# Kernel optimization log

Measured on AMD Instinct MI355X. Metric: run time of the kernel, lower is better.

## Reference

```python
import jax, jax.numpy as jnp
import numpy as np

N, D, H, E = 50000, 128, 128, 800000


def setup_inputs() -> dict:
    key = jax.random.key(0)
    ks = jax.random.split(key, 12)
    p = lambda k, shape: jax.random.normal(k, shape, dtype=jnp.float32) * 0.02
    z = lambda n: jnp.zeros((n,), jnp.float32)
    return {
        "x1": jax.random.normal(ks[0], (N, D), dtype=jnp.float32),
        "edge_index1": jax.random.randint(ks[1], (2, E), 0, N, dtype=jnp.int32),
        "x2": jax.random.normal(ks[2], (N, D), dtype=jnp.float32),
        "edge_index2": jax.random.randint(ks[3], (2, E), 0, N, dtype=jnp.int32),
        "enc_w1": p(ks[4], (D, H)), "enc_b1": z(H),
        "enc_w2": p(ks[5], (H, H)), "enc_b2": z(H),
        "conv1_w": p(ks[6], (H, H)), "conv1_b": z(H),
        "conv2_w": p(ks[7], (H, H)), "conv2_b": z(H),
        "sim_w1": p(ks[8], (4 * H, H)), "sim_b1": z(H),
        "sim_w2": p(ks[9], (H, 1)), "sim_b2": z(1),
    }


def reference(x1, edge_index1, x2, edge_index2,
              enc_w1, enc_b1, enc_w2, enc_b2,
              conv1_w, conv1_b, conv2_w, conv2_b,
              sim_w1, sim_b1, sim_w2, sim_b2):
    def gcn(x, ei, W, b):
        row, col = ei[0], ei[1]            # [E], [E]
        h = x @ W + b                      # [N, H]
        n = x.shape[0]
        deg = jax.ops.segment_sum(jnp.ones(row.shape[0], h.dtype), row, num_segments=n)
        dis = jnp.where(deg > 0, deg ** -0.5, 0.0)   # deg^-0.5, inf -> 0
        norm = dis[row] * dis[col]         # [E]
        msg = h[col] * norm[:, None]       # gather + per-edge scale, [E, H]
        return jax.ops.segment_sum(msg, row, num_segments=n)  # scatter-add

    def embed(x, ei):
        h = jax.nn.relu(x @ enc_w1 + enc_b1) @ enc_w2 + enc_b2  # encoder MLP
        h = jax.nn.relu(gcn(h, ei, conv1_w, conv1_b))
        h = jax.nn.relu(gcn(h, ei, conv2_w, conv2_b))
        return h.mean(axis=0)              # mean pooling -> [H]

    g1 = embed(x1, edge_index1)
    g2 = embed(x2, edge_index2)
    c = jnp.concatenate([g1, g2, jnp.abs(g1 - g2), g1 * g2], axis=-1)  # [4H]
    return jax.nn.relu(c @ sim_w1 + sim_b1) @ sim_w2 + sim_b2          # [1]
```

## Files before the change

kernel.cpp:

```cpp
#include <hip/hip_runtime.h>

#define HD 128

typedef _Float16 f16x8 __attribute__((ext_vector_type(8)));
typedef _Float16 f16x2 __attribute__((ext_vector_type(2)));
typedef float f32x4 __attribute__((ext_vector_type(4)));

template<bool RELU, bool SCALE, bool CVT, bool WF16>
__device__ __forceinline__ void gemm_block(
    _Float16* lds, int bi,
    const _Float16* __restrict__ Ab, const float* __restrict__ Af0,
    const float* __restrict__ Af1, const void* __restrict__ Wsrc,
    const float* __restrict__ bias, const float* __restrict__ scale,
    _Float16* __restrict__ C, int N, int Ntot) {
  const int tid = threadIdx.x;
  if (WF16) {
    const _Float16* Wf = (const _Float16*)Wsrc;
    #pragma unroll
    for (int i = 0; i < 8; ++i)
      *(float4*)&lds[tid * 8 + i * 2048] = *(const float4*)&Wf[tid * 8 + i * 2048];
  } else {
    const float* Wg = (const float*)Wsrc;
    #pragma unroll
    for (int i = 0; i < 16; ++i) {
      int flat = i * 1024 + tid * 4;
      int k = flat >> 7, n0 = flat & 127;
      float4 w4 = *(const float4*)(Wg + flat);
      int kc = k >> 5, q = (k >> 3) & 3, j = k & 7;
      float wv[4] = {w4.x, w4.y, w4.z, w4.w};
      #pragma unroll
      for (int d = 0; d < 4; ++d) {
        int n = n0 + d;
        lds[(size_t)(((n >> 4) * 4 + kc) * 64 + 16 * q + (n & 15)) * 8 + j] = (_Float16)wv[d];
      }
    }
  }
  __syncthreads();

  const int lane = tid & 63;
  const int wave = tid >> 6;
  const int n16 = lane & 15, q = lane >> 4;
  const int rowbase = bi * 128 + wave * 32;

  int arow[2];
  #pragma unroll
  for (int t = 0; t < 2; ++t) {
    int r = rowbase + 16 * t + n16;
    arow[t] = (r < Ntot) ? r : (Ntot - 1);
  }

  f32x4 acc[2][8];
  #pragma unroll
  for (int t = 0; t < 2; ++t)
    #pragma unroll
    for (int nt = 0; nt < 8; ++nt) acc[t][nt] = (f32x4){0.f, 0.f, 0.f, 0.f};

  #pragma unroll
  for (int kc = 0; kc < 4; ++kc) {
    f16x8 a[2];
    #pragma unroll
    for (int t = 0; t < 2; ++t) {
      if (CVT) {
        int r = arow[t];
        const float* src = (r < N) ? (Af0 + (size_t)r * HD) : (Af1 + (size_t)(r - N) * HD);
        float4 u0 = *(const float4*)(src + kc * 32 + q * 8);
        float4 u1 = *(const float4*)(src + kc * 32 + q * 8 + 4);
        union { _Float16 h[8]; f16x8 v; } tmp;
        tmp.h[0] = (_Float16)u0.x; tmp.h[1] = (_Float16)u0.y;
        tmp.h[2] = (_Float16)u0.z; tmp.h[3] = (_Float16)u0.w;
        tmp.h[4] = (_Float16)u1.x; tmp.h[5] = (_Float16)u1.y;
        tmp.h[6] = (_Float16)u1.z; tmp.h[7] = (_Float16)u1.w;
        a[t] = tmp.v;
      } else {
        a[t] = *(const f16x8*)(Ab + (size_t)arow[t] * HD + kc * 32 + q * 8);
      }
    }
    #pragma unroll
    for (int nt = 0; nt < 8; ++nt) {
      f16x8 b = *(const f16x8*)&lds[(size_t)((nt * 4 + kc) * 64 + lane) * 8];
      #pragma unroll
      for (int t = 0; t < 2; ++t)
        acc[t][nt] = __builtin_amdgcn_mfma_f32_16x16x32_f16(a[t], b, acc[t][nt], 0, 0, 0);
    }
  }

  float bv[8];
  #pragma unroll
  for (int nt = 0; nt < 8; ++nt) bv[nt] = bias[nt * 16 + n16];

  #pragma unroll
  for (int t = 0; t < 2; ++t) {
    #pragma unroll
    for (int r = 0; r < 4; ++r) {
      int row = rowbase + 16 * t + 4 * q + r;
      if (row < Ntot) {
        float s = SCALE ? scale[row] : 1.0f;
        #pragma unroll
        for (int nt = 0; nt < 8; ++nt) {
          float v = acc[t][nt][r] + bv[nt];
          if (RELU) v = fmaxf(v, 0.f);
          if (SCALE) v *= s;
          C[(size_t)row * HD + nt * 16 + n16] = (_Float16)v;
        }
      }
    }
  }
}

template<bool RELU, bool SCALE, bool CVT, bool WF16, int AUX, int PAT>
__global__ __launch_bounds__(256, 4) void k_fused(
    const _Float16* __restrict__ Ab, const float* __restrict__ Af0,
    const float* __restrict__ Af1, const void* __restrict__ Wsrc,
    const float* __restrict__ bias, const float* __restrict__ scale,
    _Float16* __restrict__ C, int N, int Ntot, int G, int A,
    const int* __restrict__ ei0, const int* __restrict__ ei1, int E,
    int* __restrict__ deg2, unsigned short* __restrict__ slot,
    const float* __restrict__ w1, const float* __restrict__ w2,
    const float* __restrict__ w3, _Float16* __restrict__ WfOut, int degB,
    int* __restrict__ offs, int* __restrict__ partials,
    float* __restrict__ dis, int scanB,
    unsigned short* __restrict__ csr_col, int fillB, int* __restrict__ ctr) {
  __shared__ _Float16 lds[16384];
  __shared__ int lastFlag;
  const int bi = blockIdx.x;
  const int t = threadIdx.x;

  int role, rid;
  if (PAT == 2) { role = 0; rid = bi; }
  else if (PAT == 0) {
    if (bi < 3 * G) { int k = bi / 3, r = bi % 3;
      if (r == 2) { role = 0; rid = k; } else { role = 1; rid = 2 * k + r; } }
    else { role = 1; rid = bi - G; }
  } else {
    if (bi < 3 * A) { int k = bi / 3, r = bi % 3;
      if (r == 2) { role = 1; rid = k; } else { role = 0; rid = 2 * k + r; } }
    else { role = 0; rid = bi - A; }
  }

  if (role == 0) {
    gemm_block<RELU, SCALE, CVT, WF16>(lds, rid, Ab, Af0, Af1, Wsrc,
                                       bias, scale, C, N, Ntot);
    return;
  }

  if (AUX == 1) {
    if (rid < 2 * degB) {
      int g = (rid >= degB);
      int cb = rid - g * degB;
      const int* rows = g ? ei1 : ei0;
      int* deg = deg2 + g * N;
      unsigned short* sl = slot + (size_t)g * E;
      int base = (cb * 256 + t) * 4;
      if (base + 3 < E) {
        int4 r = *(const int4*)(rows + base);
        union { unsigned short us[4]; uint2 v; } s;
        s.us[0] = (unsigned short)atomicAdd(&deg[r.x], 1);
        s.us[1] = (unsigned short)atomicAdd(&deg[r.y], 1);
        s.us[2] = (unsigned short)atomicAdd(&deg[r.z], 1);
        s.us[3] = (unsigned short)atomicAdd(&deg[r.w], 1);
        *(uint2*)(sl + base) = s.v;
      } else {
        for (int e = base; e < E; ++e)
          sl[e] = (unsigned short)atomicAdd(&deg[rows[e]], 1);
      }
    } else {
      int wb = rid - 2 * degB;
      int m = wb >> 3;
      const float* Wg = (m == 0) ? w1 : (m == 1) ? w2 : w3;
      int idx0 = (wb & 7) * 2048 + t * 8;
      float4 u0 = *(const float4*)(Wg + idx0);
      float4 u1 = *(const float4*)(Wg + idx0 + 4);
      int k = idx0 >> 7, n0 = idx0 & 127;
      int kc = k >> 5, q2 = (k >> 3) & 3, j = k & 7;
      _Float16* dst = WfOut + (size_t)m * 16384;
      float vv[8] = {u0.x, u0.y, u0.z, u0.w, u1.x, u1.y, u1.z, u1.w};
      #pragma unroll
      for (int d = 0; d < 8; ++d) {
        int n = n0 + d;
        dst[(size_t)(((n >> 4) * 4 + kc) * 64 + 16 * q2 + (n & 15)) * 8 + j] = (_Float16)vv[d];
      }
    }
  } else if (AUX == 2) {
    int* s = (int*)lds;
    int i = rid * 256 + t;
    int v = (i < Ntot) ? deg2[i] : 0;
    s[t] = v;
    __syncthreads();
    #pragma unroll
    for (int off = 1; off < 256; off <<= 1) {
      int x = (t >= off) ? s[t - off] : 0;
      __syncthreads();
      s[t] += x;
      __syncthreads();
    }
    if (i < Ntot) {
      offs[i] = s[t] - v;
      dis[i] = (v > 0) ? (1.0f / sqrtf((float)v)) : 0.0f;
    }
    if (t == 255) partials[rid] = s[255];
    __syncthreads();
    if (t == 0) {
      __threadfence();
      lastFlag = (atomicAdd(ctr, 1) == scanB - 1);
    }
    __syncthreads();
    if (lastFlag) {
      __threadfence();
      volatile int* vp = partials;
      int P = scanB;
      int v0 = (t < P) ? vp[t] : 0;
      int v1 = (t + 256 < P) ? vp[t + 256] : 0;
      __syncthreads();
      s[t] = v0;
      s[t + 256] = v1;
      __syncthreads();
      #pragma unroll
      for (int off = 1; off < 256; off <<= 1) {
        int x0 = (t >= off) ? s[t - off] : 0;
        int x1 = (t >= off) ? s[256 + t - off] : 0;
        __syncthreads();
        s[t] += x0;
        s[256 + t] += x1;
        __syncthreads();
      }
      int tot0 = s[255];
      if (t < P) partials[t] = s[t] - v0;
      if (t + 256 < P) partials[t + 256] = s[256 + t] + tot0 - v1;
    }
  } else if (AUX == 4) {
    int g = (rid >= fillB);
    int cb = rid - g * fillB;
    const int* eg = (g ? ei1 : ei0);
    const int* ob = offs + g * N;
    const unsigned short* sl = slot + (size_t)g * E;
    int gN = g * N;
    int base = (cb * 256 + t) * 4;
    if (base + 3 < E) {
      int4 r = *(const int4*)(eg + base);
      int4 c = *(const int4*)(eg + E + base);
      uint2 sv = *(const uint2*)(sl + base);
      csr_col[ob[r.x] + partials[(gN + r.x) >> 8] + (sv.x & 0xffff)] = (unsigned short)c.x;
      csr_col[ob[r.y] + partials[(gN + r.y) >> 8] + (sv.x >> 16)]    = (unsigned short)c.y;
      csr_col[ob[r.z] + partials[(gN + r.z) >> 8] + (sv.y & 0xffff)] = (unsigned short)c.z;
      csr_col[ob[r.w] + partials[(gN + r.w) >> 8] + (sv.y >> 16)]    = (unsigned short)c.w;
    } else {
      for (int e = base; e < E; ++e)
        csr_col[ob[eg[e]] + partials[(gN + eg[e]) >> 8] + sl[e]] = (unsigned short)eg[E + e];
    }
  }
}

template<bool POOL>
__global__ __launch_bounds__(256) void k_aggregate(
    const _Float16* __restrict__ T, const int* __restrict__ offs,
    const int* __restrict__ partials, const unsigned short* __restrict__ csr_col,
    const float* __restrict__ dis, _Float16* __restrict__ out,
    float* __restrict__ poolrep, int N, int Ntot, int Etot) {
  __shared__ float red[4][128];
  const int lane = threadIdx.x & 63;
  const int wave = threadIdx.x >> 6;
  const int gw = blockIdx.x * 4 + wave;
  const int sub = lane >> 4, c16 = lane & 15;

  f16x2 hacc[4];
  #pragma unroll
  for (int j = 0; j < 4; ++j) hacc[j] = (f16x2){(_Float16)0.f, (_Float16)0.f};

  if (gw < Ntot) {
    const int beg = offs[gw] + partials[gw >> 8];
    const int end = (gw + 1 == Ntot) ? Etot : (offs[gw + 1] + partials[(gw + 1) >> 8]);
    const uint4* Tg = (const uint4*)(T + (size_t)(gw >= N ? N : 0) * HD);
    for (int e = beg; e < end; e += 16) {
      uint4 v[4];
      #pragma unroll
      for (int gp = 0; gp < 4; ++gp) {
        v[gp] = make_uint4(0, 0, 0, 0);
        if (e + 4 * gp < end) {
          int eg = e + 4 * gp + sub;
          bool valid = (eg < end);
          int ce = valid ? eg : (end - 1);
          int col = csr_col[ce];
          uint4 tv = Tg[(size_t)col * 16 + c16];
          if (valid) v[gp] = tv;
        }
      }
      #pragma unroll
      for (int gp = 0; gp < 4; ++gp) {
        union { uint4 u; f16x2 h[4]; } w;
        w.u = v[gp];
        hacc[0] += w.h[0];
        hacc[1] += w.h[1];
        hacc[2] += w.h[2];
        hacc[3] += w.h[3];
      }
    }
  }

  float ax[8];
  #pragma unroll
  for (int j = 0; j < 4; ++j) {
    ax[2 * j]     = (float)hacc[j][0];
    ax[2 * j + 1] = (float)hacc[j][1];
  }
  #pragma unroll
  for (int j = 0; j < 8; ++j) {
    ax[j] += __shfl_xor(ax[j], 32, 64);
    ax[j] += __shfl_xor(ax[j], 16, 64);
  }
  float dr = (gw < Ntot) ? dis[gw] : 0.f;
  #pragma unroll
  for (int j = 0; j < 8; ++j) ax[j] = fmaxf(ax[j] * dr, 0.f);

  if (!POOL) {
    if (gw < Ntot && sub == 0) {
      union { uint4 u; _Float16 h[8]; } o;
      #pragma unroll
      for (int j = 0; j < 8; ++j) o.h[j] = (_Float16)ax[j];
      ((uint4*)out)[(size_t)gw * 16 + c16] = o.u;
    }
  } else {
    if (sub == 0) {
      *(float4*)&red[wave][c16 * 8]     = make_float4(ax[0], ax[1], ax[2], ax[3]);
      *(float4*)&red[wave][c16 * 8 + 4] = make_float4(ax[4], ax[5], ax[6], ax[7]);
    }
    __syncthreads();
    int t = threadIdx.x;
    if (t < 128) {
      float s = red[0][t] + red[1][t] + red[2][t] + red[3][t];
      int g = (blockIdx.x * 4 >= N) ? 1 : 0;
      atomicAdd(&poolrep[(size_t)((blockIdx.x & 15) * 2 + g) * 128 + t], s);
    }
  }
}

__global__ void k_final(const float* __restrict__ poolrep,
                        const float* __restrict__ W1, const float* __restrict__ b1,
                        const float* __restrict__ W2, const float* __restrict__ b2,
                        float* __restrict__ out, float invN) {
  __shared__ float cs[512];
  __shared__ float red[2];
  int t = threadIdx.x;
  float g1 = 0.f, g2 = 0.f;
  #pragma unroll
  for (int r = 0; r < 16; ++r) {
    g1 += poolrep[r * 256 + t];
    g2 += poolrep[r * 256 + 128 + t];
  }
  g1 *= invN;
  g2 *= invN;
  cs[t] = g1;
  cs[128 + t] = g2;
  cs[256 + t] = fabsf(g1 - g2);
  cs[384 + t] = g1 * g2;
  __syncthreads();
  float acc = b1[t];
  #pragma unroll 8
  for (int i = 0; i < 512; ++i) acc = fmaf(cs[i], W1[(size_t)i * HD + t], acc);
  float h = fmaxf(acc, 0.f);
  float v = h * W2[t];
  #pragma unroll
  for (int off = 32; off > 0; off >>= 1) v += __shfl_down(v, off, 64);
  if ((t & 63) == 0) red[t >> 6] = v;
  __syncthreads();
  if (t == 0) out[0] = red[0] + red[1] + b2[0];
}

extern "C" void kernel_launch(void* const* d_in, const int* in_sizes, int n_in,
                              void* d_out, int out_size, void* d_ws, size_t ws_size,
                              hipStream_t stream) {
  const float* x1     = (const float*)d_in[0];
  const int*   ei1    = (const int*)d_in[1];
  const float* x2     = (const float*)d_in[2];
  const int*   ei2    = (const int*)d_in[3];
  const float* W_in[4] = {(const float*)d_in[4], (const float*)d_in[6],
                          (const float*)d_in[8], (const float*)d_in[10]};
  const float* B_in[4] = {(const float*)d_in[5], (const float*)d_in[7],
                          (const float*)d_in[9], (const float*)d_in[11]};
  const float* sim_w1 = (const float*)d_in[12];
  const float* sim_b1 = (const float*)d_in[13];
  const float* sim_w2 = (const float*)d_in[14];
  const float* sim_b2 = (const float*)d_in[15];

  const int N = in_sizes[0] / HD;
  const int E = in_sizes[1] / 2;
  const int Ntot = 2 * N;

  _Float16* sp = (_Float16*)d_ws;
  _Float16* bufA = sp; sp += (size_t)Ntot * HD;
  _Float16* bufB = sp; sp += (size_t)Ntot * HD;
  _Float16* WfB  = sp; sp += 3 * 16384;
  float* fp = (float*)sp;
  float* dis     = fp; fp += Ntot;
  float* poolrep = fp; fp += 16 * 256;
  int* ip = (int*)fp;
  int* ctrs     = ip; ip += 8;
  int* deg2     = ip; ip += Ntot;
  int* offs     = ip; ip += Ntot;
  int* partials = ip; ip += 512;
  ip = (int*)(((uintptr_t)ip + 15) & ~(uintptr_t)15);
  unsigned short* slot = (unsigned short*)ip;
  unsigned short* csr_col = slot + 2 * (size_t)E;

  const int G = (Ntot + 127) / 128;
  const int scanB = (Ntot + 255) / 256;
  const int aggB  = (Ntot + 3) / 4;
  const int degB  = ((E + 3) / 4 + 255) / 256;
  const int fillB = degB;

  hipMemsetAsync(poolrep, 0, (16 * 256 + 8 + Ntot) * sizeof(float), stream);

  {
    int A = 2 * degB + 24;
    k_fused<true, false, true, false, 1, 0><<<A + G, 256, 0, stream>>>(
        nullptr, x1, x2, W_in[0], B_in[0], nullptr, bufA, N, Ntot, G, A,
        ei1, ei2, E, deg2, slot, W_in[1], W_in[2], W_in[3], WfB, degB,
        offs, partials, dis, scanB, csr_col, fillB, ctrs);
  }
  k_fused<false, false, false, true, 2, 1><<<scanB + G, 256, 0, stream>>>(
      bufA, nullptr, nullptr, WfB + 0 * 16384, B_in[1], nullptr, bufB, N, Ntot, G, scanB,
      ei1, ei2, E, deg2, slot, nullptr, nullptr, nullptr, nullptr, degB,
      offs, partials, dis, scanB, csr_col, fillB, ctrs);
  k_fused<false, true, false, true, 4, 0><<<2 * fillB + G, 256, 0, stream>>>(
      bufB, nullptr, nullptr, WfB + 1 * 16384, B_in[2], dis, bufA, N, Ntot, G, 2 * fillB,
      ei1, ei2, E, deg2, slot, nullptr, nullptr, nullptr, nullptr, degB,
      offs, partials, dis, scanB, csr_col, fillB, ctrs);
  k_aggregate<false><<<aggB, 256, 0, stream>>>(
      bufA, offs, partials, csr_col, dis, bufB, nullptr, N, Ntot, 2 * E);
  k_fused<false, true, false, true, 0, 2><<<G, 256, 0, stream>>>(
      bufB, nullptr, nullptr, WfB + 2 * 16384, B_in[3], dis, bufA, N, Ntot, G, 0,
      ei1, ei2, E, deg2, slot, nullptr, nullptr, nullptr, nullptr, degB,
      offs, partials, dis, scanB, csr_col, fillB, ctrs);
  k_aggregate<true><<<aggB, 256, 0, stream>>>(
      bufA, offs, partials, csr_col, dis, nullptr, poolrep, N, Ntot, 2 * E);
  k_final<<<1, 128, 0, stream>>>(poolrep, sim_w1, sim_b1, sim_w2, sim_b2,
                                 (float*)d_out, 1.0f / (float)N);
}
```

Before: 409.3 us.

## Fuse encoder MLP chain and pipeline graph halves across fused role-mapped kernels

Fuses the two encoder layers into one kernel that keeps the intermediate activations in LDS per wave, removing a full global round trip. The work is restructured so that graph 1 and graph 2 are staggered. CSR fill for one graph overlaps with aggregation of the other, and each half's GEMM overlaps with the other half's aggregation, spread over several mixed-role kernels. This adds a third activation buffer, more launches, and a fairly intricate cross-kernel dependency schedule, including assumptions such as aggB = N/4 that require N to be divisible by 4.

```diff
diff --git a/kernel.cpp b/kernel.cpp
--- a/kernel.cpp
+++ b/kernel.cpp
@@ -6,41 +6,91 @@
 typedef _Float16 f16x2 __attribute__((ext_vector_type(2)));
 typedef float f32x4 __attribute__((ext_vector_type(4)));
 
-template<bool RELU, bool SCALE, bool CVT, bool WF16>
-__device__ __forceinline__ void gemm_block(
-    _Float16* lds, int bi,
-    const _Float16* __restrict__ Ab, const float* __restrict__ Af0,
-    const float* __restrict__ Af1, const void* __restrict__ Wsrc,
+__device__ __forceinline__ void role_map(int bi, int S, int k, int& role, int& rid) {
+  int q = bi / k, rem = bi - q * k;
+  if (rem == 0 && q < S) { role = 1; rid = q; }
+  else { role = 0; int na = q + (rem ? 1 : 0); if (na > S) na = S; rid = bi - na; }
+}
+
+__global__ void k_wcvt(const float* __restrict__ w0, const float* __restrict__ w1,
+                       const float* __restrict__ w2, const float* __restrict__ w3,
+                       _Float16* __restrict__ Wf) {
+  int m = blockIdx.x >> 3;
+  const float* Wg = (m == 0) ? w0 : (m == 1) ? w1 : (m == 2) ? w2 : w3;
+  int idx0 = (blockIdx.x & 7) * 2048 + threadIdx.x * 8;
+  float4 u0 = *(const float4*)(Wg + idx0);
+  float4 u1 = *(const float4*)(Wg + idx0 + 4);
+  int k = idx0 >> 7, n0 = idx0 & 127;
+  int kc = k >> 5, q2 = (k >> 3) & 3, j = k & 7;
+  _Float16* dst = Wf + (size_t)m * 16384;
+  float vv[8] = {u0.x, u0.y, u0.z, u0.w, u1.x, u1.y, u1.z, u1.w};
+  #pragma unroll
+  for (int d = 0; d < 8; ++d) {
+    int n = n0 + d;
+    dst[(size_t)(((n >> 4) * 4 + kc) * 64 + 16 * q2 + (n & 15)) * 8 + j] = (_Float16)vv[d];
+  }
+}
+
+__device__ __forceinline__ void deg_core(int rid, int degB,
+    const int* __restrict__ ei0, const int* __restrict__ ei1, int E, int N,
+    int* __restrict__ deg2, unsigned short* __restrict__ slot) {
+  int g = (rid >= degB);
+  int cb = rid - g * degB;
+  const int* rows = g ? ei1 : ei0;
+  int* deg = deg2 + g * N;
+  unsigned short* sl = slot + (size_t)g * E;
+  int base = (cb * 256 + threadIdx.x) * 4;
+  if (base + 3 < E) {
+    int4 r = *(const int4*)(rows + base);
+    union { unsigned short us[4]; uint2 v; } s;
+    s.us[0] = (unsigned short)atomicAdd(&deg[r.x], 1);
+    s.us[1] = (unsigned short)atomicAdd(&deg[r.y], 1);
+    s.us[2] = (unsigned short)atomicAdd(&deg[r.z], 1);
+    s.us[3] = (unsigned short)atomicAdd(&deg[r.w], 1);
+    *(uint2*)(sl + base) = s.v;
+  } else {
+    for (int e = base; e < E; ++e)
+      sl[e] = (unsigned short)atomicAdd(&deg[rows[e]], 1);
+  }
+}
+
+__device__ __forceinline__ void fill_core(int rid, int g,
+    const int* __restrict__ ei0, const int* __restrict__ ei1, int E, int N,
+    const int* __restrict__ offs, const int* __restrict__ partials,
+    const unsigned short* __restrict__ slot, unsigned short* __restrict__ csr_col) {
+  const int* eg = (g ? ei1 : ei0);
+  const int* ob = offs + g * N;
+  const unsigned short* sl = slot + (size_t)g * E;
+  int gN = g * N;
+  int base = (rid * 256 + threadIdx.x) * 4;
+  if (base + 3 < E) {
+    int4 r = *(const int4*)(eg + base);
+    int4 c = *(const int4*)(eg + E + base);
+    uint2 sv = *(const uint2*)(sl + base);
+    csr_col[ob[r.x] + partials[(gN + r.x) >> 8] + (sv.x & 0xffff)] = (unsigned short)c.x;
+    csr_col[ob[r.y] + partials[(gN + r.y) >> 8] + (sv.x >> 16)]    = (unsigned short)c.y;
+    csr_col[ob[r.z] + partials[(gN + r.z) >> 8] + (sv.y & 0xffff)] = (unsigned short)c.z;
+    csr_col[ob[r.w] + partials[(gN + r.w) >> 8] + (sv.y >> 16)]    = (unsigned short)c.w;
+  } else {
+    for (int e = base; e < E; ++e)
+      csr_col[ob[eg[e]] + partials[(gN + eg[e]) >> 8] + sl[e]] = (unsigned short)eg[E + e];
+  }
+}
+
+template<bool RELU, bool SCALE>
+__device__ __forceinline__ void gemm_core(_Float16* lds, int bi, int rowOff,
+    const _Float16* __restrict__ Ab, const _Float16* __restrict__ Wf,
     const float* __restrict__ bias, const float* __restrict__ scale,
-    _Float16* __restrict__ C, int N, int Ntot) {
+    _Float16* __restrict__ C, int Ntot) {
   const int tid = threadIdx.x;
-  if (WF16) {
-    const _Float16* Wf = (const _Float16*)Wsrc;
-    #pragma unroll
-    for (int i = 0; i < 8; ++i)
-      *(float4*)&lds[tid * 8 + i * 2048] = *(const float4*)&Wf[tid * 8 + i * 2048];
-  } else {
-    const float* Wg = (const float*)Wsrc;
-    #pragma unroll
-    for (int i = 0; i < 16; ++i) {
-      int flat = i * 1024 + tid * 4;
-      int k = flat >> 7, n0 = flat & 127;
-      float4 w4 = *(const float4*)(Wg + flat);
-      int kc = k >> 5, q = (k >> 3) & 3, j = k & 7;
-      float wv[4] = {w4.x, w4.y, w4.z, w4.w};
-      #pragma unroll
-      for (int d = 0; d < 4; ++d) {
-        int n = n0 + d;
-        lds[(size_t)(((n >> 4) * 4 + kc) * 64 + 16 * q + (n & 15)) * 8 + j] = (_Float16)wv[d];
-      }
-    }
-  }
+  #pragma unroll
+  for (int i = 0; i < 8; ++i)
+    *(float4*)&lds[tid * 8 + i * 2048] = *(const float4*)&Wf[tid * 8 + i * 2048];
   __syncthreads();
 
-  const int lane = tid & 63;
-  const int wave = tid >> 6;
+  const int lane = tid & 63, wave = tid >> 6;
   const int n16 = lane & 15, q = lane >> 4;
-  const int rowbase = bi * 128 + wave * 32;
+  const int rowbase = rowOff + bi * 128 + wave * 32;
 
   int arow[2];
   #pragma unroll
@@ -48,7 +98,6 @@
     int r = rowbase + 16 * t + n16;
     arow[t] = (r < Ntot) ? r : (Ntot - 1);
   }
-
   f32x4 acc[2][8];
   #pragma unroll
   for (int t = 0; t < 2; ++t)
@@ -59,22 +108,8 @@
   for (int kc = 0; kc < 4; ++kc) {
     f16x8 a[2];
     #pragma unroll
-    for (int t = 0; t < 2; ++t) {
-      if (CVT) {
-        int r = arow[t];
-        const float* src = (r < N) ? (Af0 + (size_t)r * HD) : (Af1 + (size_t)(r - N) * HD);
-        float4 u0 = *(const float4*)(src + kc * 32 + q * 8);
-        float4 u1 = *(const float4*)(src + kc * 32 + q * 8 + 4);
-        union { _Float16 h[8]; f16x8 v; } tmp;
-        tmp.h[0] = (_Float16)u0.x; tmp.h[1] = (_Float16)u0.y;
-        tmp.h[2] = (_Float16)u0.z; tmp.h[3] = (_Float16)u0.w;
-        tmp.h[4] = (_Float16)u1.x; tmp.h[5] = (_Float16)u1.y;
-        tmp.h[6] = (_Float16)u1.z; tmp.h[7] = (_Float16)u1.w;
-        a[t] = tmp.v;
-      } else {
-        a[t] = *(const f16x8*)(Ab + (size_t)arow[t] * HD + kc * 32 + q * 8);
-      }
-    }
+    for (int t = 0; t < 2; ++t)
+      a[t] = *(const f16x8*)(Ab + (size_t)arow[t] * HD + kc * 32 + q * 8);
     #pragma unroll
     for (int nt = 0; nt < 8; ++nt) {
       f16x8 b = *(const f16x8*)&lds[(size_t)((nt * 4 + kc) * 64 + lane) * 8];
@@ -83,11 +118,9 @@
         acc[t][nt] = __builtin_amdgcn_mfma_f32_16x16x32_f16(a[t], b, acc[t][nt], 0, 0, 0);
     }
   }
-
   float bv[8];
   #pragma unroll
   for (int nt = 0; nt < 8; ++nt) bv[nt] = bias[nt * 16 + n16];
-
   #pragma unroll
   for (int t = 0; t < 2; ++t) {
     #pragma unroll
@@ -107,192 +140,142 @@
   }
 }
 
-template<bool RELU, bool SCALE, bool CVT, bool WF16, int AUX, int PAT>
-__global__ __launch_bounds__(256, 4) void k_fused(
-    const _Float16* __restrict__ Ab, const float* __restrict__ Af0,
-    const float* __restrict__ Af1, const void* __restrict__ Wsrc,
-    const float* __restrict__ bias, const float* __restrict__ scale,
-    _Float16* __restrict__ C, int N, int Ntot, int G, int A,
-    const int* __restrict__ ei0, const int* __restrict__ ei1, int E,
-    int* __restrict__ deg2, unsigned short* __restrict__ slot,
-    const float* __restrict__ w1, const float* __restrict__ w2,
-    const float* __restrict__ w3, _Float16* __restrict__ WfOut, int degB,
-    int* __restrict__ offs, int* __restrict__ partials,
-    float* __restrict__ dis, int scanB,
-    unsigned short* __restrict__ csr_col, int fillB, int* __restrict__ ctr) {
-  __shared__ _Float16 lds[16384];
-  __shared__ int lastFlag;
-  const int bi = blockIdx.x;
-  const int t = threadIdx.x;
-
-  int role, rid;
-  if (PAT == 2) { role = 0; rid = bi; }
-  else if (PAT == 0) {
-    if (bi < 3 * G) { int k = bi / 3, r = bi % 3;
-      if (r == 2) { role = 0; rid = k; } else { role = 1; rid = 2 * k + r; } }
-    else { role = 1; rid = bi - G; }
-  } else {
-    if (bi < 3 * A) { int k = bi / 3, r = bi % 3;
-      if (r == 2) { role = 1; rid = k; } else { role = 0; rid = 2 * k + r; } }
-    else { role = 0; rid = bi - A; }
-  }
-
-  if (role == 0) {
-    gemm_block<RELU, SCALE, CVT, WF16>(lds, rid, Ab, Af0, Af1, Wsrc,
-                                       bias, scale, C, N, Ntot);
-    return;
-  }
-
-  if (AUX == 1) {
-    if (rid < 2 * degB) {
-      int g = (rid >= degB);
-      int cb = rid - g * degB;
-      const int* rows = g ? ei1 : ei0;
-      int* deg = deg2 + g * N;
-      unsigned short* sl = slot + (size_t)g * E;
-      int base = (cb * 256 + t) * 4;
-      if (base + 3 < E) {
-        int4 r = *(const int4*)(rows + base);
-        union { unsigned short us[4]; uint2 v; } s;
-        s.us[0] = (unsigned short)atomicAdd(&deg[r.x], 1);
-        s.us[1] = (unsigned short)atomicAdd(&deg[r.y], 1);
-        s.us[2] = (unsigned short)atomicAdd(&deg[r.z], 1);
-        s.us[3] = (unsigned short)atomicAdd(&deg[r.w], 1);
-        *(uint2*)(sl + base) = s.v;
-      } else {
-        for (int e = base; e < E; ++e)
-          sl[e] = (unsigned short)atomicAdd(&deg[rows[e]], 1);
+__device__ __forceinline__ void chain_core(_Float16* act, int bi,
+    const float* __restrict__ x0, const float* __restrict__ x1,
+    const _Float16* __restrict__ Wf0, const _Float16* __restrict__ Wf1,
+    const float* __restrict__ b1, const float* __restrict__ b2,
+    _Float16* __restrict__ H, int N, int Ntot) {
+  const int tid = threadIdx.x;
+  const int lane = tid & 63, wave = tid >> 6;
+  const int n16 = lane & 15, q = lane >> 4;
+  const int rowbase = bi * 128 + wave * 32;
+  _Float16* wact = act + wave * 4352;
+
+  int arow[2];
+  #pragma unroll
+  for (int t = 0; t < 2; ++t) {
+    int r = rowbase + 16 * t + n16;
+    arow[t] = (r < Ntot) ? r : (Ntot - 1);
+  }
+  f32x4 acc[2][8];
+  #pragma unroll
+  for (int t = 0; t < 2; ++t)
+    #pragma unroll
+    for (int nt = 0; nt < 8; ++nt) acc[t][nt] = (f32x4){0.f, 0.f, 0.f, 0.f};
+
+  #pragma unroll
+  for (int kc = 0; kc < 4; ++kc) {
+    f16x8 a[2];
+    #pragma unroll
+    for (int t = 0; t < 2; ++t) {
+      int r = arow[t];
+      const float* src = (r < N) ? (x0 + (size_t)r * HD) : (x1 + (size_t)(r - N) * HD);
+      float4 u0 = *(const float4*)(src + kc * 32 + q * 8);
+      float4 u1 = *(const float4*)(src + kc * 32 + q * 8 + 4);
+      union { _Float16 h[8]; f16x8 v; } tmp;
+      tmp.h[0] = (_Float16)u0.x; tmp.h[1] = (_Float16)u0.y;
+      tmp.h[2] = (_Float16)u0.z; tmp.h[3] = (_Float16)u0.w;
+      tmp.h[4] = (_Float16)u1.x; tmp.h[5] = (_Float16)u1.y;
+      tmp.h[6] = (_Float16)u1.z; tmp.h[7] = (_Float16)u1.w;
+      a[t] = tmp.v;
+    }
+    #pragma unroll
+    for (int nt = 0; nt < 8; ++nt) {
+      f16x8 b = *(const f16x8*)&Wf0[(size_t)((nt * 4 + kc) * 64 + lane) * 8];
+      #pragma unroll
+      for (int t = 0; t < 2; ++t)
+        acc[t][nt] = __builtin_amdgcn_mfma_f32_16x16x32_f16(a[t], b, acc[t][nt], 0, 0, 0);
+    }
+  }
+  {
+    float bv[8];
+    #pragma unroll
+    for (int nt = 0; nt < 8; ++nt) bv[nt] = b1[nt * 16 + n16];
+    #pragma unroll
+    for (int t = 0; t < 2; ++t)
+      #pragma unroll
+      for (int r = 0; r < 4; ++r)
+        #pragma unroll
+        for (int nt = 0; nt < 8; ++nt)
+          wact[(16 * t + 4 * q + r) * 136 + nt * 16 + n16] =
+              (_Float16)fmaxf(acc[t][nt][r] + bv[nt], 0.f);
+  }
+
+  #pragma unroll
+  for (int t = 0; t < 2; ++t)
+    #pragma unroll
+    for (int nt = 0; nt < 8; ++nt) acc[t][nt] = (f32x4){0.f, 0.f, 0.f, 0.f};
+  #pragma unroll
+  for (int kc = 0; kc < 4; ++kc) {
+    f16x8 a[2];
+    #pragma unroll
+    for (int t = 0; t < 2; ++t)
+      a[t] = *(const f16x8*)&wact[(16 * t + n16) * 136 + kc * 32 + q * 8];
+    #pragma unroll
+    for (int nt = 0; nt < 8; ++nt) {
+      f16x8 b = *(const f16x8*)&Wf1[(size_t)((nt * 4 + kc) * 64 + lane) * 8];
+      #pragma unroll
+      for (int t = 0; t < 2; ++t)
+        acc[t][nt] = __builtin_amdgcn_mfma_f32_16x16x32_f16(a[t], b, acc[t][nt], 0, 0, 0);
+    }
+  }
+  {
+    float bv[8];
+    #pragma unroll
+    for (int nt = 0; nt < 8; ++nt) bv[nt] = b2[nt * 16 + n16];
+    #pragma unroll
+    for (int t = 0; t < 2; ++t)
+      #pragma unroll
+      for (int r = 0; r < 4; ++r) {
+        int row = rowbase + 16 * t + 4 * q + r;
+        if (row < Ntot)
+          #pragma unroll
+          for (int nt = 0; nt < 8; ++nt)
+            H[(size_t)row * HD + nt * 16 + n16] = (_Float16)(acc[t][nt][r] + bv[nt]);
       }
-    } else {
-      int wb = rid - 2 * degB;
-      int m = wb >> 3;
-      const float* Wg = (m == 0) ? w1 : (m == 1) ? w2 : w3;
-      int idx0 = (wb & 7) * 2048 + t * 8;
-      float4 u0 = *(const float4*)(Wg + idx0);
-      float4 u1 = *(const float4*)(Wg + idx0 + 4);
-      int k = idx0 >> 7, n0 = idx0 & 127;
-      int kc = k >> 5, q2 = (k >> 3) & 3, j = k & 7;
-      _Float16* dst = WfOut + (size_t)m * 16384;
-      float vv[8] = {u0.x, u0.y, u0.z, u0.w, u1.x, u1.y, u1.z, u1.w};
-      #pragma unroll
-      for (int d = 0; d < 8; ++d) {
-        int n = n0 + d;
-        dst[(size_t)(((n >> 4) * 4 + kc) * 64 + 16 * q2 + (n & 15)) * 8 + j] = (_Float16)vv[d];
-      }
-    }
-  } else if (AUX == 2) {
-    int* s = (int*)lds;
-    int i = rid * 256 + t;
-    int v = (i < Ntot) ? deg2[i] : 0;
-    s[t] = v;
-    __syncthreads();
-    #pragma unroll
-    for (int off = 1; off < 256; off <<= 1) {
-      int x = (t >= off) ? s[t - off] : 0;
-      __syncthreads();
-      s[t] += x;
-      __syncthreads();
-    }
-    if (i < Ntot) {
-      offs[i] = s[t] - v;
-      dis[i] = (v > 0) ? (1.0f / sqrtf((float)v)) : 0.0f;
-    }
-    if (t == 255) partials[rid] = s[255];
-    __syncthreads();
-    if (t == 0) {
-      __threadfence();
-      lastFlag = (atomicAdd(ctr, 1) == scanB - 1);
-    }
-    __syncthreads();
-    if (lastFlag) {
-      __threadfence();
-      volatile int* vp = partials;
-      int P = scanB;
-      int v0 = (t < P) ? vp[t] : 0;
-      int v1 = (t + 256 < P) ? vp[t + 256] : 0;
-      __syncthreads();
-      s[t] = v0;
-      s[t + 256] = v1;
-      __syncthreads();
-      #pragma unroll
-      for (int off = 1; off < 256; off <<= 1) {
-        int x0 = (t >= off) ? s[t - off] : 0;
-        int x1 = (t >= off) ? s[256 + t - off] : 0;
-        __syncthreads();
-        s[t] += x0;
-        s[256 + t] += x1;
-        __syncthreads();
-      }
-      int tot0 = s[255];
-      if (t < P) partials[t] = s[t] - v0;
-      if (t + 256 < P) partials[t + 256] = s[256 + t] + tot0 - v1;
-    }
-  } else if (AUX == 4) {
-    int g = (rid >= fillB);
-    int cb = rid - g * fillB;
-    const int* eg = (g ? ei1 : ei0);
-    const int* ob = offs + g * N;
-    const unsigned short* sl = slot + (size_t)g * E;
-    int gN = g * N;
-    int base = (cb * 256 + t) * 4;
-    if (base + 3 < E) {
-      int4 r = *(const int4*)(eg + base);
-      int4 c = *(const int4*)(eg + E + base);
-      uint2 sv = *(const uint2*)(sl + base);
-      csr_col[ob[r.x] + partials[(gN + r.x) >> 8] + (sv.x & 0xffff)] = (unsigned short)c.x;
-      csr_col[ob[r.y] + partials[(gN + r.y) >> 8] + (sv.x >> 16)]    = (unsigned short)c.y;
-      csr_col[ob[r.z] + partials[(gN + r.z) >> 8] + (sv.y & 0xffff)] = (unsigned short)c.z;
-      csr_col[ob[r.w] + partials[(gN + r.w) >> 8] + (sv.y >> 16)]    = (unsigned short)c.w;
-    } else {
-      for (int e = base; e < E; ++e)
-        csr_col[ob[eg[e]] + partials[(gN + eg[e]) >> 8] + sl[e]] = (unsigned short)eg[E + e];
-    }
   }
 }
 
 template<bool POOL>
-__global__ __launch_bounds__(256) void k_aggregate(
+__device__ __forceinline__ void agg_core(float* red, int rid, int nodeBase,
     const _Float16* __restrict__ T, const int* __restrict__ offs,
     const int* __restrict__ partials, const unsigned short* __restrict__ csr_col,
     const float* __restrict__ dis, _Float16* __restrict__ out,
     float* __restrict__ poolrep, int N, int Ntot, int Etot) {
-  __shared__ float red[4][128];
   const int lane = threadIdx.x & 63;
   const int wave = threadIdx.x >> 6;
-  const int gw = blockIdx.x * 4 + wave;
+  const int gw = nodeBase + rid * 4 + wave;
   const int sub = lane >> 4, c16 = lane & 15;
 
   f16x2 hacc[4];
   #pragma unroll
   for (int j = 0; j < 4; ++j) hacc[j] = (f16x2){(_Float16)0.f, (_Float16)0.f};
 
-  if (gw < Ntot) {
-    const int beg = offs[gw] + partials[gw >> 8];
-    const int end = (gw + 1 == Ntot) ? Etot : (offs[gw + 1] + partials[(gw + 1) >> 8]);
-    const uint4* Tg = (const uint4*)(T + (size_t)(gw >= N ? N : 0) * HD);
-    for (int e = beg; e < end; e += 16) {
-      uint4 v[4];
-      #pragma unroll
-      for (int gp = 0; gp < 4; ++gp) {
-        v[gp] = make_uint4(0, 0, 0, 0);
-        if (e + 4 * gp < end) {
-          int eg = e + 4 * gp + sub;
-          bool valid = (eg < end);
-          int ce = valid ? eg : (end - 1);
-          int col = csr_col[ce];
-          uint4 tv = Tg[(size_t)col * 16 + c16];
-          if (valid) v[gp] = tv;
-        }
+  const int beg = offs[gw] + partials[gw >> 8];
+  const int end = (gw + 1 == Ntot) ? Etot : (offs[gw + 1] + partials[(gw + 1) >> 8]);
+  const uint4* Tg = (const uint4*)(T + (size_t)(gw >= N ? N : 0) * HD);
+  for (int e = beg; e < end; e += 16) {
+    uint4 v[4];
+    #pragma unroll
+    for (int gp = 0; gp < 4; ++gp) {
+      v[gp] = make_uint4(0, 0, 0, 0);
+      if (e + 4 * gp < end) {
+        int eg = e + 4 * gp + sub;
+        bool valid = (eg < end);
+        int ce = valid ? eg : (end - 1);
+        int col = csr_col[ce];
+        uint4 tv = Tg[(size_t)col * 16 + c16];
+        if (valid) v[gp] = tv;
       }
-      #pragma unroll
-      for (int gp = 0; gp < 4; ++gp) {
-        union { uint4 u; f16x2 h[4]; } w;
-        w.u = v[gp];
-        hacc[0] += w.h[0];
-        hacc[1] += w.h[1];
-        hacc[2] += w.h[2];
-        hacc[3] += w.h[3];
-      }
+    }
+    #pragma unroll
+    for (int gp = 0; gp < 4; ++gp) {
+      union { uint4 u; f16x2 h[4]; } w;
+      w.u = v[gp];
+      hacc[0] += w.h[0];
+      hacc[1] += w.h[1];
+      hacc[2] += w.h[2];
+      hacc[3] += w.h[3];
     }
   }
 
@@ -307,12 +290,12 @@
     ax[j] += __shfl_xor(ax[j], 32, 64);
     ax[j] += __shfl_xor(ax[j], 16, 64);
   }
-  float dr = (gw < Ntot) ? dis[gw] : 0.f;
+  float dr = dis[gw];
   #pragma unroll
   for (int j = 0; j < 8; ++j) ax[j] = fmaxf(ax[j] * dr, 0.f);
 
   if (!POOL) {
-    if (gw < Ntot && sub == 0) {
+    if (sub == 0) {
       union { uint4 u; _Float16 h[8]; } o;
       #pragma unroll
       for (int j = 0; j < 8; ++j) o.h[j] = (_Float16)ax[j];
@@ -320,17 +303,145 @@
     }
   } else {
     if (sub == 0) {
-      *(float4*)&red[wave][c16 * 8]     = make_float4(ax[0], ax[1], ax[2], ax[3]);
-      *(float4*)&red[wave][c16 * 8 + 4] = make_float4(ax[4], ax[5], ax[6], ax[7]);
+      *(float4*)&red[wave * 128 + c16 * 8]     = make_float4(ax[0], ax[1], ax[2], ax[3]);
+      *(float4*)&red[wave * 128 + c16 * 8 + 4] = make_float4(ax[4], ax[5], ax[6], ax[7]);
     }
     __syncthreads();
     int t = threadIdx.x;
     if (t < 128) {
-      float s = red[0][t] + red[1][t] + red[2][t] + red[3][t];
-      int g = (blockIdx.x * 4 >= N) ? 1 : 0;
-      atomicAdd(&poolrep[(size_t)((blockIdx.x & 15) * 2 + g) * 128 + t], s);
-    }
-  }
+      float s = red[t] + red[128 + t] + red[256 + t] + red[384 + t];
+      int g = (nodeBase >= N) ? 1 : 0;
+      atomicAdd(&poolrep[(size_t)((rid & 15) * 2 + g) * 128 + t], s);
+    }
+  }
+}
+
+__global__ __launch_bounds__(256, 4) void k_d1(
+    const float* __restrict__ x0, const float* __restrict__ x1,
+    const _Float16* __restrict__ Wf, const float* __restrict__ b1,
+    const float* __restrict__ b2, _Float16* __restrict__ H,
+    const int* __restrict__ ei0, const int* __restrict__ ei1, int E, int N, int Ntot,
+    int* __restrict__ deg2, unsigned short* __restrict__ slot, int G, int A, int degB) {
+  __shared__ _Float16 act[4 * 4352];
+  int role, rid;
+  role_map(blockIdx.x, G, (A + G) / G, role, rid);
+  if (role == 1)
+    chain_core(act, rid, x0, x1, Wf, Wf + 16384, b1, b2, H, N, Ntot);
+  else
+    deg_core(rid, degB, ei0, ei1, E, N, deg2, slot);
+}
+
+__global__ __launch_bounds__(256, 2) void k_scan(
+    const int* __restrict__ deg2, int* __restrict__ offs, int* __restrict__ partials,
+    float* __restrict__ dis, int Ntot, int scanB, int* __restrict__ ctr) {
+  __shared__ int s[512];
+  __shared__ int lastFlag;
+  int rid = blockIdx.x, t = threadIdx.x;
+  int i = rid * 256 + t;
+  int v = (i < Ntot) ? deg2[i] : 0;
+  s[t] = v;
+  __syncthreads();
+  #pragma unroll
+  for (int off = 1; off < 256; off <<= 1) {
+    int x = (t >= off) ? s[t - off] : 0;
+    __syncthreads();
+    s[t] += x;
+    __syncthreads();
+  }
+  if (i < Ntot) {
+    offs[i] = s[t] - v;
+    dis[i] = (v > 0) ? (1.0f / sqrtf((float)v)) : 0.0f;
+  }
+  if (t == 255) partials[rid] = s[255];
+  __syncthreads();
+  if (t == 0) {
+    __threadfence();
+    lastFlag = (atomicAdd(ctr, 1) == scanB - 1);
+  }
+  __syncthreads();
+  if (lastFlag) {
+    __threadfence();
+    volatile int* vp = partials;
+    int P = scanB;
+    int v0 = (t < P) ? vp[t] : 0;
+    int v1 = (t + 256 < P) ? vp[t + 256] : 0;
+    __syncthreads();
+    s[t] = v0;
+    s[t + 256] = v1;
+    __syncthreads();
+    #pragma unroll
+    for (int off = 1; off < 256; off <<= 1) {
+      int x0 = (t >= off) ? s[t - off] : 0;
+      int x1 = (t >= off) ? s[256 + t - off] : 0;
+      __syncthreads();
+      s[t] += x0;
+      s[256 + t] += x1;
+      __syncthreads();
+    }
+    int tot0 = s[255];
+    if (t < P) partials[t] = s[t] - v0;
+    if (t + 256 < P) partials[t + 256] = s[256 + t] + tot0 - v1;
+  }
+}
+
+__global__ __launch_bounds__(256, 4) void k_gemm_fill(
+    const _Float16* __restrict__ Ain, const _Float16* __restrict__ Wf,
+    const float* __restrict__ bias, const float* __restrict__ dis,
+    _Float16* __restrict__ Cout, int Ntot, int G,
+    int fg, const int* __restrict__ ei0, const int* __restrict__ ei1, int E, int N,
+    const int* __restrict__ offs, const int* __restrict__ partials,
+    const unsigned short* __restrict__ slot, unsigned short* __restrict__ csr_col, int A) {
+  __shared__ _Float16 lds[16384];
+  int role, rid;
+  role_map(blockIdx.x, A, (A + G) / A, role, rid);
+  if (role == 1)
+    fill_core(rid, fg, ei0, ei1, E, N, offs, partials, slot, csr_col);
+  else
+    gemm_core<false, true>(lds, rid, 0, Ain, Wf, bias, dis, Cout, Ntot);
+}
+
+__global__ __launch_bounds__(256, 4) void k_agg_fill(
+    const _Float16* __restrict__ T, const int* __restrict__ offs,
+    const int* __restrict__ partials, const unsigned short* __restrict__ csr_col,
+    const float* __restrict__ dis, _Float16* __restrict__ aggOut,
+    int nodeBase, int N, int Ntot, int Etot, int nAgg,
+    int fg, const int* __restrict__ ei0, const int* __restrict__ ei1, int E,
+    const unsigned short* __restrict__ slot, unsigned short* __restrict__ csr_out, int A) {
+  int role, rid;
+  role_map(blockIdx.x, A, (nAgg + A) / A, role, rid);
+  if (role == 1)
+    fill_core(rid, fg, ei0, ei1, E, N, offs, partials, slot, csr_out);
+  else
+    agg_core<false>(nullptr, rid, nodeBase, T, offs, partials, csr_col, dis,
+                    aggOut, nullptr, N, Ntot, Etot);
+}
+
+template<bool POOL>
+__global__ __launch_bounds__(256, 4) void k_agg_gemm(
+    const _Float16* __restrict__ T, const int* __restrict__ offs,
+    const int* __restrict__ partials, const unsigned short* __restrict__ csr_col,
+    const float* __restrict__ dis, _Float16* __restrict__ aggOut,
+    float* __restrict__ poolrep, int nodeBase, int N, int Ntot, int Etot, int nAgg,
+    const _Float16* __restrict__ Ain, const _Float16* __restrict__ Wf,
+    const float* __restrict__ bias, _Float16* __restrict__ Cout, int rowOff, int G) {
+  __shared__ _Float16 lds[16384];
+  int role, rid;
+  role_map(blockIdx.x, G, (nAgg + G) / G, role, rid);
+  if (role == 1)
+    gemm_core<false, true>(lds, rid, rowOff, Ain, Wf, bias, dis, Cout, Ntot);
+  else
+    agg_core<POOL>((float*)lds, rid, nodeBase, T, offs, partials, csr_col, dis,
+                   aggOut, poolrep, N, Ntot, Etot);
+}
+
+__global__ __launch_bounds__(256) void k_agg_pool(
+    const _Float16* __restrict__ T, const int* __restrict__ offs,
+    const int* __restrict__ partials, const unsigned short* __restrict__ csr_col,
+    const float* __restrict__ dis, float* __restrict__ poolrep,
+    int nodeBase, int N, int Ntot, int Etot) {
+  __shared__ float red[512];
+  agg_core<true>(red, blockIdx.x, nodeBase, T, offs, partials, csr_col, dis,
+                 nullptr, poolrep, N, Ntot, Etot);
 }
 
 __global__ void k_final(const float* __restrict__ poolrep,
@@ -388,7 +499,8 @@
   _Float16* sp = (_Float16*)d_ws;
   _Float16* bufA = sp; sp += (size_t)Ntot * HD;
   _Float16* bufB = sp; sp += (size_t)Ntot * HD;
-  _Float16* WfB  = sp; sp += 3 * 16384;
+  _Float16* bufC = sp; sp += (size_t)Ntot * HD;
+  _Float16* WfB  = sp; sp += 4 * 16384;
   float* fp = (float*)sp;
   float* dis     = fp; fp += Ntot;
   float* poolrep = fp; fp += 16 * 256;
@@ -401,37 +513,42 @@
   unsigned short* slot = (unsigned short*)ip;
   unsigned short* csr_col = slot + 2 * (size_t)E;
 
-  const int G = (Ntot + 127) / 128;
+  const int G1    = (Ntot + 127) / 128;
+  const int Gc    = (N + 127) / 128;
   const int scanB = (Ntot + 255) / 256;
-  const int aggB  = (Ntot + 3) / 4;
+  const int aggB  = N / 4;
   const int degB  = ((E + 3) / 4 + 255) / 256;
   const int fillB = degB;
 
   hipMemsetAsync(poolrep, 0, (16 * 256 + 8 + Ntot) * sizeof(float), stream);
 
-  {
-    int A = 2 * degB + 24;
-    k_fused<true, false, true, false, 1, 0><<<A + G, 256, 0, stream>>>(
-        nullptr, x1, x2, W_in[0], B_in[0], nullptr, bufA, N, Ntot, G, A,
-        ei1, ei2, E, deg2, slot, W_in[1], W_in[2], W_in[3], WfB, degB,
-        offs, partials, dis, scanB, csr_col, fillB, ctrs);
-  }
-  k_fused<false, false, false, true, 2, 1><<<scanB + G, 256, 0, stream>>>(
-      bufA, nullptr, nullptr, WfB + 0 * 16384, B_in[1], nullptr, bufB, N, Ntot, G, scanB,
-      ei1, ei2, E, deg2, slot, nullptr, nullptr, nullptr, nullptr, degB,
-      offs, partials, dis, scanB, csr_col, fillB, ctrs);
-  k_fused<false, true, false, true, 4, 0><<<2 * fillB + G, 256, 0, stream>>>(
-      bufB, nullptr, nullptr, WfB + 1 * 16384, B_in[2], dis, bufA, N, Ntot, G, 2 * fillB,
-      ei1, ei2, E, deg2, slot, nullptr, nullptr, nullptr, nullptr, degB,
-      offs, partials, dis, scanB, csr_col, fillB, ctrs);
-  k_aggregate<false><<<aggB, 256, 0, stream>>>(
-      bufA, offs, partials, csr_col, dis, bufB, nullptr, N, Ntot, 2 * E);
-  k_fused<false, true, false, true, 0, 2><<<G, 256, 0, stream>>>(
-      bufB, nullptr, nullptr, WfB + 2 * 16384, B_in[3], dis, bufA, N, Ntot, G, 0,
-      ei1, ei2, E, deg2, slot, nullptr, nullptr, nullptr, nullptr, degB,
-      offs, partials, dis, scanB, csr_col, fillB, ctrs);
-  k_aggregate<true><<<aggB, 256, 0, stream>>>(
-      bufA, offs, partials, csr_col, dis, nullptr, poolrep, N, Ntot, 2 * E);
+  k_wcvt<<<32, 256, 0, stream>>>(W_in[0], W_in[1], W_in[2], W_in[3], WfB);
+
+  k_d1<<<2 * degB + G1, 256, 0, stream>>>(
+      x1, x2, WfB, B_in[0], B_in[1], bufA, ei1, ei2, E, N, Ntot,
+      deg2, slot, G1, 2 * degB, degB);
+
+  k_scan<<<scanB, 256, 0, stream>>>(deg2, offs, partials, dis, Ntot, scanB, ctrs);
+
+  k_gemm_fill<<<fillB + G1, 256, 0, stream>>>(
+      bufA, WfB + 2 * 16384, B_in[2], dis, bufB, Ntot, G1,
+      0, ei1, ei2, E, N, offs, partials, slot, csr_col, fillB);
+
+  k_agg_fill<<<aggB + fillB, 256, 0, stream>>>(
+      bufB, offs, partials, csr_col, dis, bufC, 0, N, Ntot, 2 * E, aggB,
+      1, ei1, ei2, E, slot, csr_col, fillB);
+
+  k_agg_gemm<false><<<aggB + Gc, 256, 0, stream>>>(
+      bufB, offs, partials, csr_col, dis, bufC, nullptr, N, N, Ntot, 2 * E, aggB,
+      bufC, WfB + 3 * 16384, B_in[3], bufA, 0, Gc);
+
+  k_agg_gemm<true><<<aggB + Gc, 256, 0, stream>>>(
+      bufA, offs, partials, csr_col, dis, nullptr, poolrep, 0, N, Ntot, 2 * E, aggB,
+      bufC, WfB + 3 * 16384, B_in[3], bufA, N, Gc);
+
+  k_agg_pool<<<aggB, 256, 0, stream>>>(
+      bufA, offs, partials, csr_col, dis, poolrep, N, N, Ntot, 2 * E);
+
   k_final<<<1, 128, 0, stream>>>(poolrep, sim_w1, sim_b1, sim_w2, sim_b2,
                                  (float*)d_out, 1.0f / (float)N);
 }
```

After: 624.3 us. +52.5%, slower.
